# Performance work log

Hardware: AMD Instinct MI355X
Metric: run time of the kernel (lower is better)

## Reference

```python
import jax, jax.numpy as jnp
import numpy as np

SIZE = 1024
N_ITER = 10
TEMP = 0.125


def setup_inputs() -> dict:
    key = jax.random.key(0)
    k1, k2 = jax.random.split(key)
    x = jax.random.normal(k1, (8, 4096, SIZE), dtype=jnp.float32)
    # weight init: identity + small gaussian noise (matches torch init)
    weight = jnp.eye(SIZE, dtype=jnp.float32) + jax.random.normal(k2, (SIZE, SIZE), dtype=jnp.float32) * 1e-05
    return {"x": x, "weight": weight}


def _sinkhorn_project(weight):
    # log-space Sinkhorn normalization: n_iter steps of symmetric row/col
    # logsumexp subtraction, then exponentiate.
    log_P = weight / TEMP
    for _ in range(N_ITER):
        r_sum = jax.nn.logsumexp(log_P, axis=-1, keepdims=True)  # [size,1]
        c_sum = jax.nn.logsumexp(log_P, axis=-2, keepdims=True)  # [1,size]
        log_P = log_P - 0.5 * (r_sum + c_sum)
    return jnp.exp(log_P)


def reference(x, weight):
    W = _sinkhorn_project(weight)          # [size, size]
    # F.linear(x, W) == x @ W.T
    return jnp.einsum('bsd,od->bso', x, W)
```

## Files before the change

kernel.cpp:

```cpp
#include <hip/hip_runtime.h>
#include <hip/hip_bf16.h>


typedef __attribute__((ext_vector_type(8))) short short8;
typedef __attribute__((ext_vector_type(4))) float f32x4;

__device__ inline unsigned int pk2(float a, float b) {
  __hip_bfloat162 h = __float22bfloat162_rn(make_float2(a, b));
  union { __hip_bfloat162 h; unsigned int u; } cv;
  cv.h = h;
  return cv.u;
}

__global__ void sinkhorn_step(const float* __restrict__ w,
                              const float* __restrict__ Rin,
                              const float* __restrict__ Cin,
                              float* __restrict__ Rout,
                              float* __restrict__ Cout,
                              int first) {
  __shared__ float red[4];
  __shared__ float4 red4[256];
  const int tid = threadIdx.x;
  const int b = blockIdx.x;
  const int lane = tid & 63, wv = tid >> 6;
  if (b < 1024) {
    const int j = tid * 4;
    float4 v = *(const float4*)(w + (size_t)b * 1024 + j);
    float4 cv = make_float4(0.f, 0.f, 0.f, 0.f);
    if (!first) cv = *(const float4*)(Cin + j);
    float s = __expf(8.f * v.x - 0.5f * cv.x) + __expf(8.f * v.y - 0.5f * cv.y)
            + __expf(8.f * v.z - 0.5f * cv.z) + __expf(8.f * v.w - 0.5f * cv.w);
    #pragma unroll
    for (int off = 32; off > 0; off >>= 1) s += __shfl_down(s, off);
    if (lane == 0) red[wv] = s;
    __syncthreads();
    if (tid == 0) {
      float t = red[0] + red[1] + red[2] + red[3];
      Rout[b] = (first ? 0.f : 0.5f * Rin[b]) + __logf(t);
    }
  } else {
    const int cb = b - 1024;
    const int c0 = cb * 16;
    const int rowg = tid >> 2, cg = tid & 3;
    const float* wp = w + (size_t)rowg * 1024 + c0 + cg * 4;
    float ax = 0.f, ay = 0.f, az = 0.f, aw = 0.f;
    #pragma unroll 4
    for (int p = 0; p < 16; ++p) {
      float4 wv4 = *(const float4*)(wp + (size_t)p * 64 * 1024);
      float rp = first ? 0.f : Rin[rowg + p * 64];
      float h = 0.5f * rp;
      ax += __expf(8.f * wv4.x - h);
      ay += __expf(8.f * wv4.y - h);
      az += __expf(8.f * wv4.z - h);
      aw += __expf(8.f * wv4.w - h);
    }
    red4[tid] = make_float4(ax, ay, az, aw);
    __syncthreads();
    if (tid < 16) {
      const int g = tid >> 2, e = tid & 3;
      float s = 0.f;
      #pragma unroll 8
      for (int q = 0; q < 64; ++q)
        s += ((const float*)&red4[q * 4 + g])[e];
      const int col = c0 + tid;
      Cout[col] = (first ? 0.f : 0.5f * Cin[col]) + __logf(s);
    }
  }
}

__global__ void make_w(const float* __restrict__ w, const float* __restrict__ R,
                       const float* __restrict__ C, unsigned short* __restrict__ Wb) {
  const int i = blockIdx.x;
  const int j = threadIdx.x * 4;
  const float r = 0.5f * R[i];
  float4 v = *(const float4*)(w + (size_t)i * 1024 + j);
  float4 cv = *(const float4*)(C + j);
  unsigned int o[2];
  o[0] = pk2(__expf(8.f * v.x - r - 0.5f * cv.x), __expf(8.f * v.y - r - 0.5f * cv.y));
  o[1] = pk2(__expf(8.f * v.z - r - 0.5f * cv.z), __expf(8.f * v.w - r - 0.5f * cv.w));
  *(uint2*)(Wb + (size_t)i * 1024 + j) = *(uint2*)o;
}

__device__ inline void swizzle_mn(int id, int& m0, int& n0) {
  m0 = ((id & 7) + ((id >> 6) << 3)) << 7;
  n0 = ((id >> 3) & 7) << 7;
}

__global__ __launch_bounds__(256) void gemm_a(const float* __restrict__ X,
                                              const unsigned short* __restrict__ Wb,
                                              float* __restrict__ out) {
  __shared__ unsigned short As[128 * 64];
  __shared__ unsigned short Bs[2][128 * 64];
  const int tid = threadIdx.x;
  const int lane = tid & 63, wave = tid >> 6;
  const int wm = wave >> 1, wn = wave & 1;
  int m0, n0;
  swizzle_mn(blockIdx.x, m0, n0);

  f32x4 acc[4][4] = {};
  const int ar = tid >> 1, ah = tid & 1;
  const float* Xrow = X + (size_t)(m0 + ar) * 1024 + ah * 32;
  const int fr = lane & 15, kq = lane >> 4;

  float4 vx[8];

#define ISSUE_B(buf, k0)                                                       \
  {                                                                            \
    _Pragma("unroll")                                                          \
    for (int is = 0; is < 4; ++is) {                                           \
      int idx = is * 256 + tid;                                                \
      int lrow = idx >> 3, lc = idx & 7;                                       \
      int g = lc ^ (lrow & 7);                                                 \
      const unsigned short* gp = Wb + (size_t)(n0 + lrow) * 1024 + (k0) + g * 8;\
      unsigned short* l = Bs[buf] + (size_t)(is * 256 + wave * 64) * 8;        \
      __builtin_amdgcn_global_load_lds(                                        \
          (const __attribute__((address_space(1))) unsigned int*)gp,           \
          (__attribute__((address_space(3))) unsigned int*)l, 16, 0, 0);       \
    }                                                                          \
  }

#define LOAD_A(k0)                                                             \
  {                                                                            \
    _Pragma("unroll")                                                          \
    for (int q = 0; q < 8; ++q) vx[q] = *(const float4*)(Xrow + (k0) + q * 4); \
  }

#define WRITE_A()                                                              \
  {                                                                            \
    _Pragma("unroll")                                                          \
    for (int q = 0; q < 4; ++q) {                                              \
      unsigned int o0 = pk2(vx[2 * q].x, vx[2 * q].y);                         \
      unsigned int o1 = pk2(vx[2 * q].z, vx[2 * q].w);                         \
      unsigned int o2 = pk2(vx[2 * q + 1].x, vx[2 * q + 1].y);                 \
      unsigned int o3 = pk2(vx[2 * q + 1].z, vx[2 * q + 1].w);                 \
      int c = ah * 4 + q;                                                      \
      int cp = c ^ (ar & 7);                                                   \
      *(uint4*)(As + (size_t)ar * 64 + cp * 8) = make_uint4(o0, o1, o2, o3);   \
    }                                                                          \
  }

  ISSUE_B(0, 0);
  LOAD_A(0);
  WRITE_A();
  ISSUE_B(1, 64);
  asm volatile("s_waitcnt vmcnt(4)" ::: "memory");
  asm volatile("s_waitcnt lgkmcnt(0)" ::: "memory");
  __builtin_amdgcn_s_barrier();
  __builtin_amdgcn_sched_barrier(0);

  int cur = 0;
  for (int t = 0; t < 16; ++t) {
    const int k0n = (t + 1) * 64;
    if (t < 15) LOAD_A(k0n);

    #pragma unroll
    for (int kk = 0; kk < 2; ++kk) {
      short8 af[4], bf[4];
      #pragma unroll
      for (int mt = 0; mt < 4; ++mt) {
        int row = wm * 64 + mt * 16 + fr;
        int cp = (kk * 4 + kq) ^ (row & 7);
        af[mt] = *(const short8*)(As + (size_t)row * 64 + cp * 8);
      }
      #pragma unroll
      for (int nt = 0; nt < 4; ++nt) {
        int row = wn * 64 + nt * 16 + fr;
        int cp = (kk * 4 + kq) ^ (row & 7);
        bf[nt] = *(const short8*)(Bs[cur] + (size_t)row * 64 + cp * 8);
      }
      #pragma unroll
      for (int mt = 0; mt < 4; ++mt)
        #pragma unroll
        for (int nt = 0; nt < 4; ++nt)
          acc[mt][nt] = __builtin_amdgcn_mfma_f32_16x16x32_bf16(af[mt], bf[nt], acc[mt][nt], 0, 0, 0);
    }
    if (t == 15) break;

    asm volatile("s_waitcnt lgkmcnt(0)" ::: "memory");
    __builtin_amdgcn_s_barrier();
    __builtin_amdgcn_sched_barrier(0);

    WRITE_A();
    if (t < 14) {
      ISSUE_B(cur, k0n + 64);
      asm volatile("s_waitcnt vmcnt(4)" ::: "memory");
    } else {
      asm volatile("s_waitcnt vmcnt(0)" ::: "memory");
    }
    asm volatile("s_waitcnt lgkmcnt(0)" ::: "memory");
    __builtin_amdgcn_s_barrier();
    __builtin_amdgcn_sched_barrier(0);
    cur ^= 1;
  }

  const int crow0 = m0 + wm * 64 + (lane >> 4) * 4;
  const int ccol0 = n0 + wn * 64 + fr;
  #pragma unroll
  for (int mt = 0; mt < 4; ++mt)
    #pragma unroll
    for (int nt = 0; nt < 4; ++nt)
      #pragma unroll
      for (int r = 0; r < 4; ++r)
        out[(size_t)(crow0 + mt * 16 + r) * 1024 + ccol0 + nt * 16] = acc[mt][nt][r];
#undef ISSUE_B
#undef LOAD_A
#undef WRITE_A
}

__global__ __launch_bounds__(256) void gemm_b(const float* __restrict__ X,
                                              const float* __restrict__ w,
                                              const float* __restrict__ R,
                                              const float* __restrict__ C,
                                              float* __restrict__ out) {
  __shared__ unsigned short As[128 * 32];
  __shared__ unsigned short Bs[128 * 32];
  const int tid = threadIdx.x;
  const int lane = tid & 63, wave = tid >> 6;
  const int wm = wave >> 1, wn = wave & 1;
  int m0, n0;
  swizzle_mn(blockIdx.x, m0, n0);

  f32x4 acc[4][4] = {};
  const int sr = tid >> 1, sk = (tid & 1) * 16;
  const float* Xrow = X + (size_t)(m0 + sr) * 1024 + sk;
  const float* Wrow = w + (size_t)(n0 + sr) * 1024 + sk;
  const float rpot = 0.5f * R[n0 + sr];

  for (int k0 = 0; k0 < 1024; k0 += 32) {
    float4 vb0 = *(const float4*)(Wrow + k0);
    float4 vb1 = *(const float4*)(Wrow + k0 + 4);
    float4 vb2 = *(const float4*)(Wrow + k0 + 8);
    float4 vb3 = *(const float4*)(Wrow + k0 + 12);
    float4 vc0 = *(const float4*)(C + k0 + sk);
    float4 vc1 = *(const float4*)(C + k0 + sk + 4);
    float4 vc2 = *(const float4*)(C + k0 + sk + 8);
    float4 vc3 = *(const float4*)(C + k0 + sk + 12);
    unsigned int pb[8];
    pb[0] = pk2(__expf(8.f * vb0.x - rpot - 0.5f * vc0.x), __expf(8.f * vb0.y - rpot - 0.5f * vc0.y));
    pb[1] = pk2(__expf(8.f * vb0.z - rpot - 0.5f * vc0.z), __expf(8.f * vb0.w - rpot - 0.5f * vc0.w));
    pb[2] = pk2(__expf(8.f * vb1.x - rpot - 0.5f * vc1.x), __expf(8.f * vb1.y - rpot - 0.5f * vc1.y));
    pb[3] = pk2(__expf(8.f * vb1.z - rpot - 0.5f * vc1.z), __expf(8.f * vb1.w - rpot - 0.5f * vc1.w));
    pb[4] = pk2(__expf(8.f * vb2.x - rpot - 0.5f * vc2.x), __expf(8.f * vb2.y - rpot - 0.5f * vc2.y));
    pb[5] = pk2(__expf(8.f * vb2.z - rpot - 0.5f * vc2.z), __expf(8.f * vb2.w - rpot - 0.5f * vc2.w));
    pb[6] = pk2(__expf(8.f * vb3.x - rpot - 0.5f * vc3.x), __expf(8.f * vb3.y - rpot - 0.5f * vc3.y));
    pb[7] = pk2(__expf(8.f * vb3.z - rpot - 0.5f * vc3.z), __expf(8.f * vb3.w - rpot - 0.5f * vc3.w));
    float4 va0 = *(const float4*)(Xrow + k0);
    float4 va1 = *(const float4*)(Xrow + k0 + 4);
    float4 va2 = *(const float4*)(Xrow + k0 + 8);
    float4 va3 = *(const float4*)(Xrow + k0 + 12);
    unsigned int pa[8];
    pa[0] = pk2(va0.x, va0.y); pa[1] = pk2(va0.z, va0.w);
    pa[2] = pk2(va1.x, va1.y); pa[3] = pk2(va1.z, va1.w);
    pa[4] = pk2(va2.x, va2.y); pa[5] = pk2(va2.z, va2.w);
    pa[6] = pk2(va3.x, va3.y); pa[7] = pk2(va3.z, va3.w);

    *(uint4*)(Bs + sr * 32 + sk)     = *(uint4*)(pb);
    *(uint4*)(Bs + sr * 32 + sk + 8) = *(uint4*)(pb + 4);
    *(uint4*)(As + sr * 32 + sk)     = *(uint4*)(pa);
    *(uint4*)(As + sr * 32 + sk + 8) = *(uint4*)(pa + 4);

    __syncthreads();

    const int kq2 = (lane >> 4) * 8;
    const int fr2 = lane & 15;
    short8 af[4], bf[4];
    #pragma unroll
    for (int t = 0; t < 4; ++t)
      af[t] = *(const short8*)(As + (wm * 64 + t * 16 + fr2) * 32 + kq2);
    #pragma unroll
    for (int t = 0; t < 4; ++t)
      bf[t] = *(const short8*)(Bs + (wn * 64 + t * 16 + fr2) * 32 + kq2);
    #pragma unroll
    for (int mt = 0; mt < 4; ++mt)
      #pragma unroll
      for (int nt = 0; nt < 4; ++nt)
        acc[mt][nt] = __builtin_amdgcn_mfma_f32_16x16x32_bf16(af[mt], bf[nt], acc[mt][nt], 0, 0, 0);

    __syncthreads();
  }

  const int crow0 = m0 + wm * 64 + (lane >> 4) * 4;
  const int ccol0 = n0 + wn * 64 + (lane & 15);
  #pragma unroll
  for (int mt = 0; mt < 4; ++mt)
    #pragma unroll
    for (int nt = 0; nt < 4; ++nt)
      #pragma unroll
      for (int r = 0; r < 4; ++r)
        out[(size_t)(crow0 + mt * 16 + r) * 1024 + ccol0 + nt * 16] = acc[mt][nt][r];
}

extern "C" void kernel_launch(void* const* d_in, const int* in_sizes, int n_in,
                              void* d_out, int out_size, void* d_ws, size_t ws_size,
                              hipStream_t stream) {
  const float* x = (const float*)d_in[0];
  const float* weight = (const float*)d_in[1];
  float* out = (float*)d_out;

  float* R0 = (float*)d_ws;
  float* C0 = R0 + 1024;
  float* R1 = C0 + 1024;
  float* C1 = R1 + 1024;
  unsigned short* Wb = (unsigned short*)(C1 + 1024);
  const size_t need_a = 16 * 1024 + 2 * 1024 * 1024;

  for (int t = 0; t < 10; ++t) {
    const float *Ri, *Ci;
    float *Ro, *Co;
    if ((t & 1) == 0) { Ri = R0; Ci = C0; Ro = R1; Co = C1; }
    else              { Ri = R1; Ci = C1; Ro = R0; Co = C0; }
    sinkhorn_step<<<1088, 256, 0, stream>>>(weight, Ri, Ci, Ro, Co, (t == 0) ? 1 : 0);
  }

  if (ws_size >= need_a) {
    make_w<<<1024, 256, 0, stream>>>(weight, R0, C0, Wb);
    gemm_a<<<2048, 256, 0, stream>>>(x, Wb, out);
  } else {
    gemm_b<<<2048, 256, 0, stream>>>(x, weight, R0, C0, out);
  }
}
```

Before: 422.7 us.

## Pre-convert X to bf16 in the Sinkhorn step and simplify the GEMM pipeline

When the workspace is large enough, the first Sinkhorn step also launches extra blocks that convert X from fp32 to bf16 into the workspace. A new GEMM then streams both operands straight into LDS with global_load_lds, replacing the in-loop fp32 load and convert of X that the old kernel repeated for every N tile. The row logsumexp is restructured to one wave per row across 256 blocks, which removes the shared-memory reduction. In exchange, the GEMMs drop double buffering in favour of a single LDS buffer with __syncthreads, which can expose load latency, and the conversion adds a full extra pass over X.

```diff
diff --git a/kernel.cpp b/kernel.cpp
--- a/kernel.cpp
+++ b/kernel.cpp
@@ -17,29 +17,32 @@
                               const float* __restrict__ Cin,
                               float* __restrict__ Rout,
                               float* __restrict__ Cout,
-                              int first) {
-  __shared__ float red[4];
+                              int first,
+                              const float* __restrict__ X,
+                              unsigned short* __restrict__ Xb,
+                              int do_cvt) {
   __shared__ float4 red4[256];
   const int tid = threadIdx.x;
   const int b = blockIdx.x;
   const int lane = tid & 63, wv = tid >> 6;
-  if (b < 1024) {
-    const int j = tid * 4;
-    float4 v = *(const float4*)(w + (size_t)b * 1024 + j);
-    float4 cv = make_float4(0.f, 0.f, 0.f, 0.f);
-    if (!first) cv = *(const float4*)(Cin + j);
-    float s = __expf(8.f * v.x - 0.5f * cv.x) + __expf(8.f * v.y - 0.5f * cv.y)
-            + __expf(8.f * v.z - 0.5f * cv.z) + __expf(8.f * v.w - 0.5f * cv.w);
+  if (b < 256) {
+    const int row = 4 * b + wv;
+    const float* rp = w + (size_t)row * 1024 + lane * 16;
+    float s = 0.f;
+    #pragma unroll
+    for (int q = 0; q < 4; ++q) {
+      float4 v4 = *(const float4*)(rp + q * 4);
+      float4 c4 = make_float4(0.f, 0.f, 0.f, 0.f);
+      if (!first) c4 = *(const float4*)(Cin + lane * 16 + q * 4);
+      s += __expf(8.f * v4.x - 0.5f * c4.x) + __expf(8.f * v4.y - 0.5f * c4.y)
+         + __expf(8.f * v4.z - 0.5f * c4.z) + __expf(8.f * v4.w - 0.5f * c4.w);
+    }
     #pragma unroll
     for (int off = 32; off > 0; off >>= 1) s += __shfl_down(s, off);
-    if (lane == 0) red[wv] = s;
-    __syncthreads();
-    if (tid == 0) {
-      float t = red[0] + red[1] + red[2] + red[3];
-      Rout[b] = (first ? 0.f : 0.5f * Rin[b]) + __logf(t);
-    }
-  } else {
-    const int cb = b - 1024;
+    if (lane == 0)
+      Rout[row] = (first ? 0.f : 0.5f * Rin[row]) + __logf(s);
+  } else if (b < 320) {
+    const int cb = b - 256;
     const int c0 = cb * 16;
     const int rowg = tid >> 2, cg = tid & 3;
     const float* wp = w + (size_t)rowg * 1024 + c0 + cg * 4;
@@ -65,6 +68,18 @@
       const int col = c0 + tid;
       Cout[col] = (first ? 0.f : 0.5f * Cin[col]) + __logf(s);
     }
+  } else if (do_cvt) {
+    const size_t idx0 = (size_t)(b - 320) * 256 + tid;
+    #pragma unroll
+    for (int it = 0; it < 8; ++it) {
+      size_t e = (it * 524288ull + idx0) * 8;
+      float4 a = *(const float4*)(X + e);
+      float4 c = *(const float4*)(X + e + 4);
+      uint4 o;
+      o.x = pk2(a.x, a.y); o.y = pk2(a.z, a.w);
+      o.z = pk2(c.x, c.y); o.w = pk2(c.z, c.w);
+      *(uint4*)(Xb + e) = o;
+    }
   }
 }
 
@@ -86,11 +101,11 @@
   n0 = ((id >> 3) & 7) << 7;
 }
 
-__global__ __launch_bounds__(256) void gemm_a(const float* __restrict__ X,
-                                              const unsigned short* __restrict__ Wb,
-                                              float* __restrict__ out) {
+__global__ __launch_bounds__(256) void gemm_bb(const unsigned short* __restrict__ Xb,
+                                               const unsigned short* __restrict__ Wb,
+                                               float* __restrict__ out) {
   __shared__ unsigned short As[128 * 64];
-  __shared__ unsigned short Bs[2][128 * 64];
+  __shared__ unsigned short Bs[128 * 64];
   const int tid = threadIdx.x;
   const int lane = tid & 63, wave = tid >> 6;
   const int wm = wave >> 1, wn = wave & 1;
@@ -98,60 +113,27 @@
   swizzle_mn(blockIdx.x, m0, n0);
 
   f32x4 acc[4][4] = {};
-  const int ar = tid >> 1, ah = tid & 1;
-  const float* Xrow = X + (size_t)(m0 + ar) * 1024 + ah * 32;
   const int fr = lane & 15, kq = lane >> 4;
 
-  float4 vx[8];
-
-#define ISSUE_B(buf, k0)                                                       \
-  {                                                                            \
-    _Pragma("unroll")                                                          \
-    for (int is = 0; is < 4; ++is) {                                           \
-      int idx = is * 256 + tid;                                                \
-      int lrow = idx >> 3, lc = idx & 7;                                       \
-      int g = lc ^ (lrow & 7);                                                 \
-      const unsigned short* gp = Wb + (size_t)(n0 + lrow) * 1024 + (k0) + g * 8;\
-      unsigned short* l = Bs[buf] + (size_t)(is * 256 + wave * 64) * 8;        \
-      __builtin_amdgcn_global_load_lds(                                        \
-          (const __attribute__((address_space(1))) unsigned int*)gp,           \
-          (__attribute__((address_space(3))) unsigned int*)l, 16, 0, 0);       \
-    }                                                                          \
-  }
-
-#define LOAD_A(k0)                                                             \
-  {                                                                            \
-    _Pragma("unroll")                                                          \
-    for (int q = 0; q < 8; ++q) vx[q] = *(const float4*)(Xrow + (k0) + q * 4); \
-  }
-
-#define WRITE_A()                                                              \
-  {                                                                            \
-    _Pragma("unroll")                                                          \
-    for (int q = 0; q < 4; ++q) {                                              \
-      unsigned int o0 = pk2(vx[2 * q].x, vx[2 * q].y);                         \
-      unsigned int o1 = pk2(vx[2 * q].z, vx[2 * q].w);                         \
-      unsigned int o2 = pk2(vx[2 * q + 1].x, vx[2 * q + 1].y);                 \
-      unsigned int o3 = pk2(vx[2 * q + 1].z, vx[2 * q + 1].w);                 \
-      int c = ah * 4 + q;                                                      \
-      int cp = c ^ (ar & 7);                                                   \
-      *(uint4*)(As + (size_t)ar * 64 + cp * 8) = make_uint4(o0, o1, o2, o3);   \
-    }                                                                          \
-  }
-
-  ISSUE_B(0, 0);
-  LOAD_A(0);
-  WRITE_A();
-  ISSUE_B(1, 64);
-  asm volatile("s_waitcnt vmcnt(4)" ::: "memory");
-  asm volatile("s_waitcnt lgkmcnt(0)" ::: "memory");
-  __builtin_amdgcn_s_barrier();
-  __builtin_amdgcn_sched_barrier(0);
-
-  int cur = 0;
   for (int t = 0; t < 16; ++t) {
-    const int k0n = (t + 1) * 64;
-    if (t < 15) LOAD_A(k0n);
+    const int k0 = t * 64;
+    #pragma unroll
+    for (int is = 0; is < 4; ++is) {
+      int idx = is * 256 + tid;
+      int lrow = idx >> 3;
+      int g = (idx & 7) ^ (lrow & 7);
+      const unsigned short* ga = Xb + (size_t)(m0 + lrow) * 1024 + k0 + g * 8;
+      const unsigned short* gb = Wb + (size_t)(n0 + lrow) * 1024 + k0 + g * 8;
+      unsigned short* la = As + (size_t)(is * 256 + wave * 64) * 8;
+      unsigned short* lb = Bs + (size_t)(is * 256 + wave * 64) * 8;
+      __builtin_amdgcn_global_load_lds(
+          (const __attribute__((address_space(1))) unsigned int*)ga,
+          (__attribute__((address_space(3))) unsigned int*)la, 16, 0, 0);
+      __builtin_amdgcn_global_load_lds(
+          (const __attribute__((address_space(1))) unsigned int*)gb,
+          (__attribute__((address_space(3))) unsigned int*)lb, 16, 0, 0);
+    }
+    __syncthreads();
 
     #pragma unroll
     for (int kk = 0; kk < 2; ++kk) {
@@ -166,7 +148,7 @@
       for (int nt = 0; nt < 4; ++nt) {
         int row = wn * 64 + nt * 16 + fr;
         int cp = (kk * 4 + kq) ^ (row & 7);
-        bf[nt] = *(const short8*)(Bs[cur] + (size_t)row * 64 + cp * 8);
+        bf[nt] = *(const short8*)(Bs + (size_t)row * 64 + cp * 8);
       }
       #pragma unroll
       for (int mt = 0; mt < 4; ++mt)
@@ -174,23 +156,7 @@
         for (int nt = 0; nt < 4; ++nt)
           acc[mt][nt] = __builtin_amdgcn_mfma_f32_16x16x32_bf16(af[mt], bf[nt], acc[mt][nt], 0, 0, 0);
     }
-    if (t == 15) break;
-
-    asm volatile("s_waitcnt lgkmcnt(0)" ::: "memory");
-    __builtin_amdgcn_s_barrier();
-    __builtin_amdgcn_sched_barrier(0);
-
-    WRITE_A();
-    if (t < 14) {
-      ISSUE_B(cur, k0n + 64);
-      asm volatile("s_waitcnt vmcnt(4)" ::: "memory");
-    } else {
-      asm volatile("s_waitcnt vmcnt(0)" ::: "memory");
-    }
-    asm volatile("s_waitcnt lgkmcnt(0)" ::: "memory");
-    __builtin_amdgcn_s_barrier();
-    __builtin_amdgcn_sched_barrier(0);
-    cur ^= 1;
+    __syncthreads();
   }
 
   const int crow0 = m0 + wm * 64 + (lane >> 4) * 4;
@@ -202,9 +168,82 @@
       #pragma unroll
       for (int r = 0; r < 4; ++r)
         out[(size_t)(crow0 + mt * 16 + r) * 1024 + ccol0 + nt * 16] = acc[mt][nt][r];
-#undef ISSUE_B
-#undef LOAD_A
-#undef WRITE_A
+}
+
+__global__ __launch_bounds__(256) void gemm_f(const float* __restrict__ X,
+                                              const unsigned short* __restrict__ Wb,
+                                              float* __restrict__ out) {
+  __shared__ unsigned short As[128 * 64];
+  __shared__ unsigned short Bs[128 * 64];
+  const int tid = threadIdx.x;
+  const int lane = tid & 63, wave = tid >> 6;
+  const int wm = wave >> 1, wn = wave & 1;
+  int m0, n0;
+  swizzle_mn(blockIdx.x, m0, n0);
+
+  f32x4 acc[4][4] = {};
+  const int ar = tid >> 1, ah = tid & 1;
+  const float* Xrow = X + (size_t)(m0 + ar) * 1024 + ah * 32;
+  const int fr = lane & 15, kq = lane >> 4;
+
+  for (int t = 0; t < 16; ++t) {
+    const int k0 = t * 64;
+    #pragma unroll
+    for (int is = 0; is < 4; ++is) {
+      int idx = is * 256 + tid;
+      int lrow = idx >> 3;
+      int g = (idx & 7) ^ (lrow & 7);
+      const unsigned short* gb = Wb + (size_t)(n0 + lrow) * 1024 + k0 + g * 8;
+      unsigned short* lb = Bs + (size_t)(is * 256 + wave * 64) * 8;
+      __builtin_amdgcn_global_load_lds(
+          (const __attribute__((address_space(1))) unsigned int*)gb,
+          (__attribute__((address_space(3))) unsigned int*)lb, 16, 0, 0);
+    }
+    #pragma unroll
+    for (int q = 0; q < 4; ++q) {
+      float4 a = *(const float4*)(Xrow + k0 + q * 8);
+      float4 c = *(const float4*)(Xrow + k0 + q * 8 + 4);
+      uint4 o;
+      o.x = pk2(a.x, a.y); o.y = pk2(a.z, a.w);
+      o.z = pk2(c.x, c.y); o.w = pk2(c.z, c.w);
+      int cp = (ah * 4 + q) ^ (ar & 7);
+      *(uint4*)(As + (size_t)ar * 64 + cp * 8) = o;
+    }
+    __syncthreads();
+
+    #pragma unroll
+    for (int kk = 0; kk < 2; ++kk) {
+      short8 af[4], bf[4];
+      #pragma unroll
+      for (int mt = 0; mt < 4; ++mt) {
+        int row = wm * 64 + mt * 16 + fr;
+        int cp = (kk * 4 + kq) ^ (row & 7);
+        af[mt] = *(const short8*)(As + (size_t)row * 64 + cp * 8);
+      }
+      #pragma unroll
+      for (int nt = 0; nt < 4; ++nt) {
+        int row = wn * 64 + nt * 16 + fr;
+        int cp = (kk * 4 + kq) ^ (row & 7);
+        bf[nt] = *(const short8*)(Bs + (size_t)row * 64 + cp * 8);
+      }
+      #pragma unroll
+      for (int mt = 0; mt < 4; ++mt)
+        #pragma unroll
+        for (int nt = 0; nt < 4; ++nt)
+          acc[mt][nt] = __builtin_amdgcn_mfma_f32_16x16x32_bf16(af[mt], bf[nt], acc[mt][nt], 0, 0, 0);
+    }
+    __syncthreads();
+  }
+
+  const int crow0 = m0 + wm * 64 + (lane >> 4) * 4;
+  const int ccol0 = n0 + wn * 64 + fr;
+  #pragma unroll
+  for (int mt = 0; mt < 4; ++mt)
+    #pragma unroll
+    for (int nt = 0; nt < 4; ++nt)
+      #pragma unroll
+      for (int r = 0; r < 4; ++r)
+        out[(size_t)(crow0 + mt * 16 + r) * 1024 + ccol0 + nt * 16] = acc[mt][nt][r];
 }
 
 __global__ __launch_bounds__(256) void gemm_b(const float* __restrict__ X,
@@ -302,19 +341,27 @@
   float* R1 = C0 + 1024;
   float* C1 = R1 + 1024;
   unsigned short* Wb = (unsigned short*)(C1 + 1024);
-  const size_t need_a = 16 * 1024 + 2 * 1024 * 1024;
+  unsigned short* Xb = Wb + (size_t)1024 * 1024;
+  const size_t need_small = 16 * 1024 + 2 * 1024 * 1024;
+  const size_t need_big = need_small + (size_t)32768 * 1024 * 2;
+  const int big = (ws_size >= need_big) ? 1 : 0;
+  const int small_ok = (ws_size >= need_small) ? 1 : 0;
 
   for (int t = 0; t < 10; ++t) {
     const float *Ri, *Ci;
     float *Ro, *Co;
     if ((t & 1) == 0) { Ri = R0; Ci = C0; Ro = R1; Co = C1; }
     else              { Ri = R1; Ci = C1; Ro = R0; Co = C0; }
-    sinkhorn_step<<<1088, 256, 0, stream>>>(weight, Ri, Ci, Ro, Co, (t == 0) ? 1 : 0);
-  }
-
-  if (ws_size >= need_a) {
+    const int cvt = (t == 0 && big) ? 1 : 0;
+    const int grid = cvt ? 2368 : 320;
+    sinkhorn_step<<<grid, 256, 0, stream>>>(weight, Ri, Ci, Ro, Co,
+                                            (t == 0) ? 1 : 0, x, Xb, cvt);
+  }
+
+  if (small_ok) {
     make_w<<<1024, 256, 0, stream>>>(weight, R0, C0, Wb);
-    gemm_a<<<2048, 256, 0, stream>>>(x, Wb, out);
+    if (big) gemm_bb<<<2048, 256, 0, stream>>>(Xb, Wb, out);
+    else     gemm_f<<<2048, 256, 0, stream>>>(x, Wb, out);
   } else {
     gemm_b<<<2048, 256, 0, stream>>>(x, weight, R0, C0, out);
   }
```

New measurement: 377.5 us. -10.7%, faster.
